# Optimization experiments

Hardware: AMD Instinct MI355X
Metric: run time of the kernel (lower is better)

The kernel has to match this reference:

```python
import jax, jax.numpy as jnp
import numpy as np

T, B, IN, H, L = 512, 256, 64, 128, 5  # seq, batch, in_dim, hidden, layers


def _lstm_layer(x_seq, W_ih, W_hh, b_ih, b_hh):
    # x_seq: [T, B, D]; W_ih: [4H, D]; W_hh: [4H, H]; biases: [4H]
    # Precompute input contribution for all timesteps (big GEMM, compute-dense)
    pre = jnp.einsum('tbd,gd->tbg', x_seq, W_ih) + b_ih + b_hh  # [T, B, 4H]
    h0 = jnp.zeros((x_seq.shape[1], W_hh.shape[1]), x_seq.dtype)
    c0 = h0

    def step(carry, p):
        h, c = carry
        gates = p + h @ W_hh.T  # [B, 4H], PyTorch gate order i,f,g,o
        i, f, g, o = jnp.split(gates, 4, axis=-1)
        i = jax.nn.sigmoid(i)
        f = jax.nn.sigmoid(f)
        g = jnp.tanh(g)
        o = jax.nn.sigmoid(o)
        c = f * c + i * g
        h = o * jnp.tanh(c)
        return (h, c), h

    _, hs = jax.lax.scan(step, (h0, c0), pre)
    return hs  # [T, B, H]


def setup_inputs() -> dict:
    key = jax.random.key(0)
    ks = jax.random.split(key, 6)
    s = 1.0 / np.sqrt(H)  # PyTorch LSTM init scale
    return {
        'x': jax.random.normal(ks[0], (T, B, IN), jnp.float32),
        'W_ih0': jax.random.uniform(ks[1], (4 * H, IN), jnp.float32, -s, s),
        'W_ih_rest': jax.random.uniform(ks[2], (L - 1, 4 * H, H), jnp.float32, -s, s),
        'W_hh': jax.random.uniform(ks[3], (L, 4 * H, H), jnp.float32, -s, s),
        'b_ih': jax.random.uniform(ks[4], (L, 4 * H), jnp.float32, -s, s),
        'b_hh': jax.random.uniform(ks[5], (L, 4 * H), jnp.float32, -s, s),
    }


def reference(x, W_ih0, W_ih_rest, W_hh, b_ih, b_hh):
    # 5-layer stacked LSTM, eval mode (inter-layer dropout inactive).
    h = _lstm_layer(x, W_ih0, W_hh[0], b_ih[0], b_hh[0])
    for l in range(1, L):  # fixed small layer loop
        h = _lstm_layer(h, W_ih_rest[l - 1], W_hh[l], b_ih[l], b_hh[l])
    return h  # [T, B, H]
```

## Files before the change

kernel.cpp:

```cpp
#include <hip/hip_runtime.h>


typedef unsigned short ushort_t;
typedef unsigned int uint_t;
typedef unsigned long long ull_t;
typedef __attribute__((ext_vector_type(8))) short short8;
typedef __attribute__((ext_vector_type(4))) float floatx4;
typedef __attribute__((ext_vector_type(2))) float floatx2;

#define T_STEPS 512
#define BATCH   256
#define HID     128
#define NL      5
#define NBG     16
#define RING_R  64
#define PRIME   18
#define FLAG_STRIDE 16
#define SLOT_U  (BATCH * HID / 2)
#define RING_U  ((size_t)RING_R * SLOT_U)
#define WS_NEED (8192 + 4 * RING_U * 4)
#define LDS_BYTES 43552

__device__ __forceinline__ ushort_t f2bf(float f) {
  unsigned int u = __float_as_uint(f);
  u += 0x7FFF + ((u >> 16) & 1);
  return (ushort_t)(u >> 16);
}
__device__ __forceinline__ float sigm(float x) {
  float e = __builtin_amdgcn_exp2f(-1.442695041f * x);
  return __builtin_amdgcn_rcpf(1.0f + e);
}
__device__ __forceinline__ float tanh_(float x) {
  float e = __builtin_amdgcn_exp2f(-2.885390082f * x);
  float s = __builtin_amdgcn_rcpf(1.0f + e);
  return __builtin_fmaf(2.0f, s, -1.0f);
}
__device__ __forceinline__ int flag_ld(const int* p) {
  return __hip_atomic_load(p, __ATOMIC_RELAXED, __HIP_MEMORY_SCOPE_AGENT);
}
__device__ __forceinline__ ull_t ring_ld8(const uint_t* base, int tid) {
  return __hip_atomic_load((const ull_t*)base + tid, __ATOMIC_RELAXED,
                           __HIP_MEMORY_SCOPE_AGENT);
}
__device__ __forceinline__ void ring_st8(uint_t* base, int tid, ull_t v) {
  __hip_atomic_store((ull_t*)base + tid, v, __ATOMIC_RELAXED,
                     __HIP_MEMORY_SCOPE_AGENT);
}

__global__ void init_flags(int* flags) {
  int i = blockIdx.x * 256 + threadIdx.x;
  if (i < NL * NBG * FLAG_STRIDE)
    __hip_atomic_store(&flags[i], 0, __ATOMIC_RELAXED,
                       __HIP_MEMORY_SCOPE_AGENT);
}

template <int KIN, bool SRC_F32, bool RING_OUT>
__device__ __forceinline__ void lstm_stage(
    unsigned char* lds,
    const float* xf32,
    const uint_t* ring_in,
    const float* __restrict__ Wih, const float* __restrict__ Whh,
    const float* __restrict__ bih, const float* __restrict__ bhh,
    uint_t* ring_out,
    float* out_f32,
    int* up_flag, int* down_flag, int* my_flag, int bg)
{
  constexpr int KX = KIN / 32, KT = KX + 4;
  constexpr int XS = KIN + 8;
  constexpr int HS = 128 + 8;

  typedef ushort_t (*XT)[16][XS];
  typedef ushort_t (*HT)[16][HS];
  XT Xr = (XT)lds;
  HT Hr = (HT)(lds + (size_t)8 * 16 * XS * 2);
  int* upm = (int*)(lds + (size_t)8 * 16 * XS * 2 + (size_t)2 * 16 * HS * 2);
  int* dnm = upm + 4;

  const int tid  = threadIdx.x;
  const int wave = tid >> 6;
  const int lane = tid & 63;
  const int col  = lane & 15;
  const int quad = lane >> 4;
  const int j    = wave * 16 + col;
  const int frow = tid >> 5;
  const int fc   = tid & 31;

  for (int i = tid; i < 2 * 16 * HS; i += 512) (&Hr[0][0][0])[i] = 0;
  if (tid == 0) {
#pragma unroll
    for (int i = 0; i < 4; ++i) { upm[i] = 0; dnm[i] = 0; }
  }

  short8 wf[4][KT];
#pragma unroll
  for (int nt = 0; nt < 4; ++nt) {
    int n = nt * 128 + j;
#pragma unroll
    for (int kt = 0; kt < KX; ++kt) {
      const float* p = Wih + n * KIN + kt * 32 + quad * 8;
      short8 w;
#pragma unroll
      for (int e = 0; e < 8; ++e) w[e] = (short)f2bf(p[e]);
      wf[nt][kt] = w;
    }
#pragma unroll
    for (int kt = 0; kt < 4; ++kt) {
      const float* p = Whh + n * 128 + kt * 32 + quad * 8;
      short8 w;
#pragma unroll
      for (int e = 0; e < 8; ++e) w[e] = (short)f2bf(p[e]);
      wf[nt][KX + kt] = w;
    }
  }
  const float bi  = bih[j]       + bhh[j];
  const float bf_ = bih[128 + j] + bhh[128 + j];
  const float bgi = bih[256 + j] + bhh[256 + j];
  const float bo  = bih[384 + j] + bhh[384 + j];

  floatx4 c = {0.f, 0.f, 0.f, 0.f};
  int nf;
  int pu = 0, pd = 0;
  ull_t pf = 0;
  floatx2 pxf = {0.f, 0.f};

  __syncthreads();

  if constexpr (!SRC_F32) {
    int v = 0;
    while ((v = flag_ld(up_flag)) < PRIME) __builtin_amdgcn_s_sleep(1);
    asm volatile("" ::: "memory");
    if (tid == 0) {
#pragma unroll
      for (int i = 0; i < 4; ++i) upm[i] = v;
      pu = v;
    }
    ull_t pr[8];
#pragma unroll
    for (int s = 0; s < 8; ++s)
      pr[s] = ring_ld8(ring_in + (size_t)s * SLOT_U + bg * 1024, tid);
#pragma unroll
    for (int s = 0; s < 8; ++s)
      *(ull_t*)(&Xr[s][frow][fc * 4]) = pr[s];
  } else {
    floatx2 pr[8];
#pragma unroll
    for (int s = 0; s < 8; ++s)
      pr[s] = *(const floatx2*)(xf32 +
                                ((size_t)s * BATCH + bg * 16 + frow) * 64 +
                                fc * 2);
#pragma unroll
    for (int s = 0; s < 8; ++s)
      *(uint_t*)(&Xr[s][frow][fc * 2]) =
          (uint_t)f2bf(pr[s][0]) | ((uint_t)f2bf(pr[s][1]) << 16);
  }
  nf = 8;
  asm volatile("s_waitcnt lgkmcnt(0)\n\ts_barrier" ::: "memory");

  for (int t = 0; t < T_STEPS; ++t) {
    if ((t & 3) == 0 && t >= 4) {
      asm volatile("s_waitcnt vmcnt(0)\n\ts_barrier" ::: "memory");
      if (tid == 0)
        __hip_atomic_store(my_flag, t - 1, __ATOMIC_RELAXED,
                           __HIP_MEMORY_SCOPE_AGENT);
    }
    const int am = upm[t & 3];
    const int dn = dnm[t & 3];

    if constexpr (!SRC_F32) {
      if (nf == t) {
        while (flag_ld(up_flag) < t + 1) __builtin_amdgcn_s_sleep(1);
        asm volatile("" ::: "memory");
        ull_t e = ring_ld8(
            ring_in + (size_t)(t & (RING_R - 1)) * SLOT_U + bg * 1024, tid);
        *(ull_t*)(&Xr[t & 7][frow][fc * 4]) = e;
        nf = t + 1;
        asm volatile("s_waitcnt lgkmcnt(0)\n\ts_barrier" ::: "memory");
      }
    }

    if constexpr (RING_OUT) {
      if (t >= 1) {
        const int s = t - 1;
        if (s - dn > RING_R - 16) {
          while (s - flag_ld(down_flag) > RING_R - 16)
            __builtin_amdgcn_s_sleep(1);
          asm volatile("" ::: "memory");
        }
        ull_t h8 = *(const ull_t*)(&Hr[t & 1][frow][fc * 4]);
        ring_st8(ring_out + (size_t)(s & (RING_R - 1)) * SLOT_U + bg * 1024,
                 tid, h8);
      }
    }

    bool dofetch;
    if constexpr (SRC_F32) {
      dofetch = (nf <= t + 7) && (nf < T_STEPS);
      if (dofetch)
        pxf = *(const floatx2*)(xf32 +
                                ((size_t)nf * BATCH + bg * 16 + frow) * 64 +
                                fc * 2);
    } else {
      dofetch = (nf <= t + 7) && (nf < T_STEPS) && (am >= nf + 1);
      if (dofetch)
        pf = ring_ld8(
            ring_in + (size_t)(nf & (RING_R - 1)) * SLOT_U + bg * 1024, tid);
    }

    short8 af[KT];
#pragma unroll
    for (int kt = 0; kt < KX; ++kt)
      af[kt] = *(const short8*)(&Xr[t & 7][col][kt * 32 + quad * 8]);
#pragma unroll
    for (int kt = 0; kt < 4; ++kt)
      af[KX + kt] = *(const short8*)(&Hr[t & 1][col][kt * 32 + quad * 8]);
    floatx4 a0 = {0, 0, 0, 0}, a1 = {0, 0, 0, 0}, a2 = {0, 0, 0, 0},
            a3 = {0, 0, 0, 0};
#pragma unroll
    for (int kt = 0; kt < KT; ++kt) {
      short8 a = af[kt];
      a0 = __builtin_amdgcn_mfma_f32_16x16x32_bf16(a, wf[0][kt], a0, 0, 0, 0);
      a1 = __builtin_amdgcn_mfma_f32_16x16x32_bf16(a, wf[1][kt], a1, 0, 0, 0);
      a2 = __builtin_amdgcn_mfma_f32_16x16x32_bf16(a, wf[2][kt], a2, 0, 0, 0);
      a3 = __builtin_amdgcn_mfma_f32_16x16x32_bf16(a, wf[3][kt], a3, 0, 0, 0);
    }

    if (tid == 0) {
      if constexpr (!SRC_F32) {
        upm[(t + 2) & 3] = pu;
        pu = flag_ld(up_flag);
      }
      if constexpr (RING_OUT) {
        dnm[(t + 2) & 3] = pd;
        pd = flag_ld(down_flag);
      }
    }

    ushort_t (*wr)[HS] = Hr[(t & 1) ^ 1];
#pragma unroll
    for (int r = 0; r < 4; ++r) {
      float iv = sigm(a0[r] + bi);
      float fv = sigm(a1[r] + bf_);
      float gv = tanh_(a2[r] + bgi);
      float ov = sigm(a3[r] + bo);
      float cn = __builtin_fmaf(fv, c[r], iv * gv);
      c[r] = cn;
      float hv = ov * tanh_(cn);
      wr[quad * 4 + r][j] = f2bf(hv);
      if constexpr (!RING_OUT) {
        out_f32[((size_t)t * BATCH + bg * 16 + quad * 4 + r) * HID + j] = hv;
      }
    }

    if (dofetch) {
      if constexpr (SRC_F32)
        *(uint_t*)(&Xr[nf & 7][frow][fc * 2]) =
            (uint_t)f2bf(pxf[0]) | ((uint_t)f2bf(pxf[1]) << 16);
      else
        *(ull_t*)(&Xr[nf & 7][frow][fc * 4]) = pf;
      ++nf;
    }

    asm volatile("s_waitcnt lgkmcnt(0)\n\ts_barrier" ::: "memory");
  }

  if constexpr (RING_OUT) {
    const int s = T_STEPS - 1;
    while (s - flag_ld(down_flag) > RING_R - 16) __builtin_amdgcn_s_sleep(1);
    asm volatile("" ::: "memory");
    ull_t h8 = *(const ull_t*)(&Hr[T_STEPS & 1][frow][fc * 4]);
    ring_st8(ring_out + (size_t)(s & (RING_R - 1)) * SLOT_U + bg * 1024, tid,
             h8);
  }
  asm volatile("s_waitcnt vmcnt(0)\n\ts_barrier" ::: "memory");
  if (tid == 0)
    __hip_atomic_store(my_flag, T_STEPS, __ATOMIC_RELAXED,
                       __HIP_MEMORY_SCOPE_AGENT);
}

__global__ __launch_bounds__(512) void lstm_pipe(
    const float* x, const float* Wih0, const float* WihR,
    const float* Whh, const float* bih, const float* bhh,
    float* out, uint_t* ring, int* flags)
{
  __shared__ __align__(16) unsigned char lds_raw[LDS_BYTES];
  const int l  = blockIdx.x >> 4;
  const int bg = blockIdx.x & 15;
  int* mine = flags + (l * NBG + bg) * FLAG_STRIDE;
  int* up   = (l > 0) ? flags + ((l - 1) * NBG + bg) * FLAG_STRIDE : nullptr;
  int* down = (l < 4) ? flags + ((l + 1) * NBG + bg) * FLAG_STRIDE : nullptr;

  if (l == 0) {
    lstm_stage<64, true, true>(lds_raw, x, nullptr, Wih0, Whh, bih, bhh,
                               ring, nullptr, up, down, mine, bg);
  } else if (l < 4) {
    lstm_stage<128, false, true>(lds_raw, nullptr,
                                 ring + (size_t)(l - 1) * RING_U,
                                 WihR + (size_t)(l - 1) * 512 * 128,
                                 Whh + (size_t)l * 512 * 128,
                                 bih + l * 512, bhh + l * 512,
                                 ring + (size_t)l * RING_U, nullptr,
                                 up, down, mine, bg);
  } else {
    lstm_stage<128, false, false>(lds_raw, nullptr,
                                  ring + (size_t)3 * RING_U,
                                  WihR + (size_t)3 * 512 * 128,
                                  Whh + (size_t)4 * 512 * 128,
                                  bih + 4 * 512, bhh + 4 * 512,
                                  nullptr, out, up, nullptr, mine, bg);
  }
}

template <int KIN>
__global__ __launch_bounds__(512) void lstm_layer(
    const float* xin, float* hout,
    const float* __restrict__ Wih, const float* __restrict__ Whh,
    const float* __restrict__ bih, const float* __restrict__ bhh)
{
  constexpr int KX = KIN / 32, KT = KX + 4;
  constexpr int AW = KIN + 128, AS = AW + 8;
  constexpr int NSTG = 16 * KIN / 4;

  const int bg = blockIdx.x, tid = threadIdx.x;
  const int wave = tid >> 6, lane = tid & 63;
  const int col = lane & 15, quad = lane >> 4;
  const int j = wave * 16 + col;

  __shared__ __align__(16) ushort_t Ah[2][16][AS];
  for (int i = tid; i < 2 * 16 * AS; i += 512) (&Ah[0][0][0])[i] = 0;

  short8 wf[4][KT];
#pragma unroll
  for (int nt = 0; nt < 4; ++nt) {
    int n = nt * 128 + j;
#pragma unroll
    for (int kt = 0; kt < KX; ++kt) {
      const float* p = Wih + n * KIN + kt * 32 + quad * 8;
      short8 w;
#pragma unroll
      for (int e = 0; e < 8; ++e) w[e] = (short)f2bf(p[e]);
      wf[nt][kt] = w;
    }
#pragma unroll
    for (int kt = 0; kt < 4; ++kt) {
      const float* p = Whh + n * 128 + kt * 32 + quad * 8;
      short8 w;
#pragma unroll
      for (int e = 0; e < 8; ++e) w[e] = (short)f2bf(p[e]);
      wf[nt][KX + kt] = w;
    }
  }
  const float bi  = bih[j]       + bhh[j];
  const float bf_ = bih[128 + j] + bhh[128 + j];
  const float bgi = bih[256 + j] + bhh[256 + j];
  const float bo  = bih[384 + j] + bhh[384 + j];

  floatx4 c = {0.f, 0.f, 0.f, 0.f};
  const int srow = tid / (KIN / 4), scol = (tid % (KIN / 4)) * 4;
  floatx4 xv = {0.f, 0.f, 0.f, 0.f};
  auto stage_load = [&](int t) {
    if (tid < NSTG && t < T_STEPS)
      xv = *(const floatx4*)(xin + (size_t)(t * BATCH + bg * 16 + srow) * KIN + scol);
  };
  auto stage_store = [&](int t, ushort_t (*buf)[AS]) {
    if (tid < NSTG && t < T_STEPS) {
#pragma unroll
      for (int e = 0; e < 4; ++e) buf[srow][scol + e] = f2bf(xv[e]);
    }
  };
  __syncthreads();
  stage_load(0); stage_store(0, Ah[0]); stage_load(1);
  __syncthreads();

  for (int t = 0; t < T_STEPS; ++t) {
    ushort_t (*rd)[AS] = Ah[t & 1];
    ushort_t (*wr)[AS] = Ah[(t & 1) ^ 1];
    short8 af[KT];
#pragma unroll
    for (int kt = 0; kt < KT; ++kt)
      af[kt] = *(const short8*)(&rd[col][kt * 32 + quad * 8]);
    floatx4 a0 = {0, 0, 0, 0}, a1 = {0, 0, 0, 0}, a2 = {0, 0, 0, 0},
            a3 = {0, 0, 0, 0};
#pragma unroll
    for (int kt = 0; kt < KT; ++kt) {
      short8 a = af[kt];
      a0 = __builtin_amdgcn_mfma_f32_16x16x32_bf16(a, wf[0][kt], a0, 0, 0, 0);
      a1 = __builtin_amdgcn_mfma_f32_16x16x32_bf16(a, wf[1][kt], a1, 0, 0, 0);
      a2 = __builtin_amdgcn_mfma_f32_16x16x32_bf16(a, wf[2][kt], a2, 0, 0, 0);
      a3 = __builtin_amdgcn_mfma_f32_16x16x32_bf16(a, wf[3][kt], a3, 0, 0, 0);
    }
    stage_store(t + 1, wr);
    stage_load(t + 2);
    size_t obase = (size_t)(t * BATCH + bg * 16) * HID + j;
#pragma unroll
    for (int r = 0; r < 4; ++r) {
      int row = quad * 4 + r;
      float iv = sigm(a0[r] + bi);
      float fv = sigm(a1[r] + bf_);
      float gv = tanh_(a2[r] + bgi);
      float ov = sigm(a3[r] + bo);
      float cn = __builtin_fmaf(fv, c[r], iv * gv);
      c[r] = cn;
      float hv = ov * tanh_(cn);
      wr[row][KIN + j] = f2bf(hv);
      hout[obase + (size_t)row * HID] = hv;
    }
    __syncthreads();
  }
}

extern "C" void kernel_launch(void* const* d_in, const int* in_sizes, int n_in,
                              void* d_out, int out_size, void* d_ws,
                              size_t ws_size, hipStream_t stream) {
  const float* x    = (const float*)d_in[0];
  const float* Wih0 = (const float*)d_in[1];
  const float* WihR = (const float*)d_in[2];
  const float* Whh  = (const float*)d_in[3];
  const float* bih  = (const float*)d_in[4];
  const float* bhh  = (const float*)d_in[5];
  float* out = (float*)d_out;

  if (ws_size >= WS_NEED) {
    int* flags = (int*)d_ws;
    uint_t* ring = (uint_t*)((char*)d_ws + 8192);
    init_flags<<<(NL * NBG * FLAG_STRIDE + 255) / 256, 256, 0, stream>>>(flags);
    lstm_pipe<<<NL * NBG, 512, 0, stream>>>(x, Wih0, WihR, Whh, bih, bhh,
                                            out, ring, flags);
  } else {
    lstm_layer<64><<<16, 512, 0, stream>>>(x, out, Wih0, Whh, bih, bhh);
    for (int l = 1; l < 5; ++l)
      lstm_layer<128><<<16, 512, 0, stream>>>(
          out, out, WihR + (size_t)(l - 1) * 512 * 128,
          Whh + (size_t)l * 512 * 128, bih + l * 512, bhh + l * 512);
  }
}
```

Before: 888.4 us.

## Batch layer-input prefetch into four-step groups and raise ring priming depth

Replaces the per-step adaptive input prefetch (one ring or fp32 load per step, with an optional blocking fetch when the LDS buffer runs dry) with a grouped scheme. Every four steps the kernel loads four future timesteps into registers, then writes them into the 8-slot LDS input buffer at the next group boundary, reusing the existing group barrier. Upstream-flag waiting moves to once per group and requires the producer layer to be 12 steps ahead, and the initial priming threshold rises from 18 to 24 steps. This removes per-step branching and stalls inside the recurrent loop, at the cost of more registers and a larger required lag between layers, which can lengthen the cross-layer pipeline fill.

```diff
diff --git a/kernel.cpp b/kernel.cpp
--- a/kernel.cpp
+++ b/kernel.cpp
@@ -14,7 +14,7 @@
 #define NL      5
 #define NBG     16
 #define RING_R  64
-#define PRIME   18
+#define PRIME   24
 #define FLAG_STRIDE 16
 #define SLOT_U  (BATCH * HID / 2)
 #define RING_U  ((size_t)RING_R * SLOT_U)
@@ -118,10 +118,9 @@
   const float bo  = bih[384 + j] + bhh[384 + j];
 
   floatx4 c = {0.f, 0.f, 0.f, 0.f};
-  int nf;
   int pu = 0, pd = 0;
-  ull_t pf = 0;
-  floatx2 pxf = {0.f, 0.f};
+  ull_t  pf4[4];
+  floatx2 px4[4];
 
   __syncthreads();
 
@@ -153,30 +152,52 @@
       *(uint_t*)(&Xr[s][frow][fc * 2]) =
           (uint_t)f2bf(pr[s][0]) | ((uint_t)f2bf(pr[s][1]) << 16);
   }
-  nf = 8;
   asm volatile("s_waitcnt lgkmcnt(0)\n\ts_barrier" ::: "memory");
 
   for (int t = 0; t < T_STEPS; ++t) {
-    if ((t & 3) == 0 && t >= 4) {
-      asm volatile("s_waitcnt vmcnt(0)\n\ts_barrier" ::: "memory");
-      if (tid == 0)
-        __hip_atomic_store(my_flag, t - 1, __ATOMIC_RELAXED,
-                           __HIP_MEMORY_SCOPE_AGENT);
-    }
-    const int am = upm[t & 3];
+    if ((t & 3) == 0) {
+      if (t >= 4) {
+        asm volatile("s_waitcnt vmcnt(0)\n\ts_barrier" ::: "memory");
+        if (tid == 0)
+          __hip_atomic_store(my_flag, t - 1, __ATOMIC_RELAXED,
+                             __HIP_MEMORY_SCOPE_AGENT);
+#pragma unroll
+        for (int g = 0; g < 4; ++g) {
+          const int s = t + 4 + g;
+          if (s < T_STEPS) {
+            if constexpr (SRC_F32)
+              *(uint_t*)(&Xr[s & 7][frow][fc * 2]) =
+                  (uint_t)f2bf(px4[g][0]) | ((uint_t)f2bf(px4[g][1]) << 16);
+            else
+              *(ull_t*)(&Xr[s & 7][frow][fc * 4]) = pf4[g];
+          }
+        }
+      }
+      if (t + 8 < T_STEPS) {
+        if constexpr (!SRC_F32) {
+          int need = t + 12;
+          if (need > T_STEPS) need = T_STEPS;
+          if (upm[t & 3] < need) {
+            while (flag_ld(up_flag) < need) __builtin_amdgcn_s_sleep(1);
+          }
+        }
+        asm volatile("" ::: "memory");
+#pragma unroll
+        for (int g = 0; g < 4; ++g) {
+          const int s = t + 8 + g;
+          if (s < T_STEPS) {
+            if constexpr (SRC_F32)
+              px4[g] = *(const floatx2*)(
+                  xf32 + ((size_t)s * BATCH + bg * 16 + frow) * 64 + fc * 2);
+            else
+              pf4[g] = ring_ld8(
+                  ring_in + (size_t)(s & (RING_R - 1)) * SLOT_U + bg * 1024,
+                  tid);
+          }
+        }
+      }
+    }
     const int dn = dnm[t & 3];
-
-    if constexpr (!SRC_F32) {
-      if (nf == t) {
-        while (flag_ld(up_flag) < t + 1) __builtin_amdgcn_s_sleep(1);
-        asm volatile("" ::: "memory");
-        ull_t e = ring_ld8(
-            ring_in + (size_t)(t & (RING_R - 1)) * SLOT_U + bg * 1024, tid);
-        *(ull_t*)(&Xr[t & 7][frow][fc * 4]) = e;
-        nf = t + 1;
-        asm volatile("s_waitcnt lgkmcnt(0)\n\ts_barrier" ::: "memory");
-      }
-    }
 
     if constexpr (RING_OUT) {
       if (t >= 1) {
@@ -192,20 +213,6 @@
       }
     }
 
-    bool dofetch;
-    if constexpr (SRC_F32) {
-      dofetch = (nf <= t + 7) && (nf < T_STEPS);
-      if (dofetch)
-        pxf = *(const floatx2*)(xf32 +
-                                ((size_t)nf * BATCH + bg * 16 + frow) * 64 +
-                                fc * 2);
-    } else {
-      dofetch = (nf <= t + 7) && (nf < T_STEPS) && (am >= nf + 1);
-      if (dofetch)
-        pf = ring_ld8(
-            ring_in + (size_t)(nf & (RING_R - 1)) * SLOT_U + bg * 1024, tid);
-    }
-
     short8 af[KT];
 #pragma unroll
     for (int kt = 0; kt < KX; ++kt)
@@ -249,15 +256,6 @@
       if constexpr (!RING_OUT) {
         out_f32[((size_t)t * BATCH + bg * 16 + quad * 4 + r) * HID + j] = hv;
       }
-    }
-
-    if (dofetch) {
-      if constexpr (SRC_F32)
-        *(uint_t*)(&Xr[nf & 7][frow][fc * 2]) =
-            (uint_t)f2bf(pxf[0]) | ((uint_t)f2bf(pxf[1]) << 16);
-      else
-        *(ull_t*)(&Xr[nf & 7][frow][fc * 4]) = pf;
-      ++nf;
     }
 
     asm volatile("s_waitcnt lgkmcnt(0)\n\ts_barrier" ::: "memory");
```

Result: no change. 896.2 us (+0.9%).
